# Optimization experiments

Hardware: AMD Instinct MI355X
Metric: run time of the kernel (lower is better)

The kernel has to match this reference:

```python
import jax, jax.numpy as jnp
import numpy as np

B, T, D, H = 2, 2048, 1024, 16
DK = D // H


def setup_inputs() -> dict:
    key = jax.random.key(0)
    ks = jax.random.split(key, 13)
    s = 1.0 / np.sqrt(D)
    return {
        "q": jax.random.normal(ks[0], (B, T, D), jnp.float32),
        "k": jax.random.normal(ks[1], (B, T, D), jnp.float32),
        "v": jax.random.normal(ks[2], (B, T, D), jnp.float32),
        "mask": jax.random.randint(ks[3], (B, T, T), 0, 2, jnp.int32),
        "Wq": jax.random.normal(ks[4], (D, D), jnp.float32) * s,
        "bq": jax.random.normal(ks[5], (D,), jnp.float32) * s,
        "Wk": jax.random.normal(ks[6], (D, D), jnp.float32) * s,
        "bk": jax.random.normal(ks[7], (D,), jnp.float32) * s,
        "Wv": jax.random.normal(ks[8], (D, D), jnp.float32) * s,
        "bv": jax.random.normal(ks[9], (D,), jnp.float32) * s,
        "Wo": jax.random.normal(ks[10], (D, D), jnp.float32) * s,
        "bo": jax.random.normal(ks[11], (D,), jnp.float32) * s,
    }


def reference(q, k, v, mask, Wq, bq, Wk, bk, Wv, bv, Wo, bo):
    # Linear projections (torch Linear: x @ W.T + b), split into heads.
    Q = (q @ Wq.T + bq).reshape(B, T, H, DK).transpose(0, 2, 1, 3)  # [B,H,Tq,dk]
    K = (k @ Wk.T + bk).reshape(B, T, H, DK).transpose(0, 2, 1, 3)
    V = (v @ Wv.T + bv).reshape(B, T, H, DK).transpose(0, 2, 1, 3)
    scores = jnp.einsum("bhqd,bhkd->bhqk", Q, K) / jnp.sqrt(jnp.float32(DK))
    # 3-dim mask path: mask==0 -> -1e9, broadcast over heads.
    scores = jnp.where(mask[:, None, :, :] == 0, jnp.float32(-1e9), scores)
    attn = jax.nn.softmax(scores, axis=-1)
    out = jnp.einsum("bhqk,bhkd->bhqd", attn, V)  # [B,H,Tq,dk]
    out = out.transpose(0, 2, 1, 3).reshape(B, T, D)
    return out @ Wo.T + bo
```

## Files before the change

### kernel.cpp

```cpp
#include <hip/hip_runtime.h>
#include <cstdint>
#include <cstddef>

#define TSEQ 2048
#define DMOD 1024
#define NHEAD 16
#define NBATCH 2
#define MT (NBATCH * TSEQ)
#define LOG2E 1.44269504088896340736f

typedef __attribute__((ext_vector_type(8))) __bf16 bf16x8;
typedef __attribute__((ext_vector_type(4))) float f32x4;
typedef __attribute__((ext_vector_type(8))) unsigned short u16x8;
typedef __attribute__((ext_vector_type(4))) unsigned short u16x4;
typedef __attribute__((ext_vector_type(4))) uint32_t u32x4;

__device__ __forceinline__ unsigned short f2bf(float f) {
  uint32_t u = __builtin_bit_cast(uint32_t, f);
  u += 0x7fffu + ((u >> 16) & 1u);
  return (unsigned short)(u >> 16);
}

__device__ __forceinline__ uint32_t cvt_pk_bf16(float a, float b) {
  uint32_t r;
  asm("v_cvt_pk_bf16_f32 %0, %1, %2" : "=v"(r) : "v"(a), "v"(b));
  return r;
}

__device__ __forceinline__ void gload_lds16(const void* g, const void* l) {
  auto gp = (const __attribute__((address_space(1))) uint32_t*)((uintptr_t)g);
  auto lp = (__attribute__((address_space(3))) uint32_t*)((uintptr_t)l);
  __builtin_amdgcn_global_load_lds(gp, lp, 16, 0, 0);
}

__global__ __launch_bounds__(256) void cvt_in(const float* __restrict__ q,
                                              const float* __restrict__ k,
                                              const float* __restrict__ v,
                                              unsigned short* __restrict__ dst) {
  const int y = blockIdx.y;
  const float* s = y == 0 ? q : (y == 1 ? k : v);
  const size_t i = ((size_t)blockIdx.x * 256 + threadIdx.x) * 4;
  const float4 t = *(const float4*)(s + i);
  u16x4 o;
  o[0] = f2bf(t.x); o[1] = f2bf(t.y); o[2] = f2bf(t.z); o[3] = f2bf(t.w);
  *(u16x4*)(dst + (size_t)y * MT * DMOD + i) = o;
}

__global__ __launch_bounds__(256) void cvt_w(const float* __restrict__ w0,
                                             const float* __restrict__ w1,
                                             const float* __restrict__ w2,
                                             const float* __restrict__ w3,
                                             unsigned short* __restrict__ dst) {
  const int y = blockIdx.y;
  const float* s = y == 0 ? w0 : (y == 1 ? w1 : (y == 2 ? w2 : w3));
  const size_t i = ((size_t)blockIdx.x * 256 + threadIdx.x) * 4;
  const float4 t = *(const float4*)(s + i);
  u16x4 o;
  o[0] = f2bf(t.x); o[1] = f2bf(t.y); o[2] = f2bf(t.z); o[3] = f2bf(t.w);
  *(u16x4*)(dst + (size_t)y * DMOD * DMOD + i) = o;
}

__global__ __launch_bounds__(256) void mask_bits(const int* __restrict__ m,
                                                 uint32_t* __restrict__ bits) {
  const int wg = (blockIdx.x * 256 + threadIdx.x) >> 6;
  const int lane = threadIdx.x & 63;
  const int v = m[(size_t)wg * 64 + lane];
  const unsigned long long b = __ballot(v != 0);
  if (lane == 0) *(uint2*)(bits + (size_t)wg * 2) = make_uint2((uint32_t)b, (uint32_t)(b >> 32));
}

__device__ __forceinline__ void store_c(unsigned short* C, size_t idx, float v) { C[idx] = f2bf(v); }
__device__ __forceinline__ void store_c(float* C, size_t idx, float v) { C[idx] = v; }

template <typename OT>
__global__ __launch_bounds__(256) void gemm_bt(const unsigned short* __restrict__ A0,
                                               const unsigned short* __restrict__ A1,
                                               const unsigned short* __restrict__ A2,
                                               const unsigned short* __restrict__ W0,
                                               const unsigned short* __restrict__ W1,
                                               const unsigned short* __restrict__ W2,
                                               const float* __restrict__ b0,
                                               const float* __restrict__ b1,
                                               const float* __restrict__ b2,
                                               OT* __restrict__ C0, OT* __restrict__ C1, OT* __restrict__ C2,
                                               float s0, float s1, float s2) {
  const int z = blockIdx.z;
  const unsigned short* A  = z == 0 ? A0 : (z == 1 ? A1 : A2);
  const unsigned short* Bw = z == 0 ? W0 : (z == 1 ? W1 : W2);
  const float* bias = z == 0 ? b0 : (z == 1 ? b1 : b2);
  OT* C = z == 0 ? C0 : (z == 1 ? C1 : C2);
  const float scale = z == 0 ? s0 : (z == 1 ? s1 : s2);

  __shared__ alignas(16) unsigned short As[128 * 32];
  __shared__ alignas(16) unsigned short Bs[128 * 32];
  const int tid = threadIdx.x;
  const int wid = tid >> 6;
  const int lane = tid & 63;
  const int lo = lane & 15, hi = lane >> 4;
  const int m0 = blockIdx.x * 128, n0 = blockIdx.y * 128;
  const int wr = wid >> 1, wc = wid & 1;
  f32x4 acc[4][4] = {};

  for (int k0 = 0; k0 < DMOD; k0 += 32) {
    __syncthreads();
#pragma unroll
    for (int i = 0; i < 2; ++i) {
      const int chunk = i * 256 + tid;
      const int row = chunk >> 2, c = chunk & 3;
      const int wb = (i * 256 + wid * 64) * 16;
      gload_lds16(A + (size_t)(m0 + row) * DMOD + k0 + c * 8, (const char*)As + wb);
      gload_lds16(Bw + (size_t)(n0 + row) * DMOD + k0 + c * 8, (const char*)Bs + wb);
    }
    __syncthreads();
    bf16x8 af[4], bfr[4];
#pragma unroll
    for (int m = 0; m < 4; ++m)
      af[m] = *(const bf16x8*)((const char*)As + (wr * 64 + m * 16 + lo) * 64 + hi * 16);
#pragma unroll
    for (int n = 0; n < 4; ++n)
      bfr[n] = *(const bf16x8*)((const char*)Bs + (wc * 64 + n * 16 + lo) * 64 + hi * 16);
#pragma unroll
    for (int m = 0; m < 4; ++m)
#pragma unroll
      for (int n = 0; n < 4; ++n)
        acc[m][n] = __builtin_amdgcn_mfma_f32_16x16x32_bf16(af[m], bfr[n], acc[m][n], 0, 0, 0);
  }

#pragma unroll
  for (int n = 0; n < 4; ++n) {
    const int col = n0 + wc * 64 + n * 16 + lo;
    const float bv = bias[col];
#pragma unroll
    for (int m = 0; m < 4; ++m) {
      const int row = m0 + wr * 64 + m * 16 + hi * 4;
#pragma unroll
      for (int r = 0; r < 4; ++r)
        store_c(C, (size_t)(row + r) * DMOD + col, (acc[m][n][r] + bv) * scale);
    }
  }
}

__global__ __launch_bounds__(256) void transpose_v(const unsigned short* __restrict__ Vp,
                                                   unsigned short* __restrict__ Vt) {
  __shared__ alignas(16) unsigned short tile[64][72];
  const int tid = threadIdx.x;
  const int bt0 = blockIdx.x * 64;
  const int h = blockIdx.y;
  const int b = bt0 >> 11;
  const int t0 = bt0 & (TSEQ - 1);
#pragma unroll
  for (int i = 0; i < 2; ++i) {
    const int chunk = i * 256 + tid;
    const int row = chunk >> 3, c = chunk & 7;
    *(uint4*)((char*)&tile[row][0] + c * 16) =
        *(const uint4*)(Vp + (size_t)(bt0 + row) * DMOD + h * 64 + c * 8);
  }
  __syncthreads();
#pragma unroll
  for (int i = 0; i < 2; ++i) {
    const int chunk = i * 256 + tid;
    const int dk = chunk >> 3, c = chunk & 7;
    u16x8 o;
#pragma unroll
    for (int j = 0; j < 8; ++j) {
      const int x = c * 8 + j;
      const int kl = (x & 32) | ((x & 24) >> 1) | ((x & 4) << 2) | (x & 3);
      o[j] = tile[kl][dk];
    }
    *(u16x8*)(Vt + ((size_t)(b * NHEAD + h) * 64 + dk) * TSEQ + t0 + c * 8) = o;
  }
}

__global__ __launch_bounds__(512, 4) void attn_kernel(const unsigned short* __restrict__ Qp,
                                                      const unsigned short* __restrict__ Kp,
                                                      const unsigned short* __restrict__ Vt,
                                                      const uint32_t* __restrict__ mbits,
                                                      unsigned short* __restrict__ AO) {
  __shared__ alignas(16) unsigned short Ks[2][128 * 64];
  __shared__ alignas(16) unsigned short Vs[2][64 * 128];
  const int tid = threadIdx.x;
  const int w = tid >> 6, lane = tid & 63;
  const int lo = lane & 15, hi = lane >> 4;
  const int f = blockIdx.x;
  const int swz = (f & 7) * 64 + (f >> 3);
  const int q0 = (swz & 15) * 128;
  const int h = (swz >> 4) & 15;
  const int b = swz >> 8;

  bf16x8 qf[2];
  {
    const unsigned short* qsrc =
        Qp + (size_t)(b * TSEQ + q0 + w * 16 + lo) * DMOD + h * 64 + hi * 8;
    qf[0] = *(const bf16x8*)qsrc;
    qf[1] = *(const bf16x8*)(qsrc + 32);
  }

  bf16x8 ones;
  {
    u32x4 od;
    od[0] = 0x3F803F80u; od[1] = 0x3F803F80u; od[2] = 0x3F803F80u; od[3] = 0x3F803F80u;
    ones = __builtin_bit_cast(bf16x8, od);
  }

  f32x4 o_acc[4] = {};
  f32x4 l_acc = {};

  const size_t kbase = (size_t)(b * TSEQ) * DMOD + h * 64;
  const size_t vbase = (size_t)(b * NHEAD + h) * 64 * TSEQ;
  const uint32_t* mrow = mbits + (size_t)(b * TSEQ + q0 + w * 16 + lo) * 64;

  auto stage = [&](int buf, int kt2) {
#pragma unroll
    for (int i = 0; i < 2; ++i) {
      const int chunk = i * 512 + tid;
      const int wb = chunk * 16;
      {
        const int row = chunk >> 3, c = (chunk & 7) ^ (row & 7);
        gload_lds16(Kp + kbase + (size_t)(kt2 * 128 + row) * DMOD + c * 8,
                    (const char*)Ks[buf] + wb);
      }
      {
        const int row = chunk >> 4, c = (chunk & 15) ^ (row & 7);
        gload_lds16(Vt + vbase + (size_t)row * TSEQ + kt2 * 128 + c * 8,
                    (const char*)Vs[buf] + wb);
      }
    }
  };

  const int NT = TSEQ / 128;
  stage(0, 0);
  uint4 mw = *(const uint4*)(mrow);
  __syncthreads();

  for (int kt = 0; kt < NT; ++kt) {
    const int cur = kt & 1;
    uint4 mw_next = mw;
    if (kt + 1 < NT) {
      stage(cur ^ 1, kt + 1);
      mw_next = *(const uint4*)(mrow + (kt + 1) * 4);
    }

    const char* ksb = (const char*)Ks[cur];
    f32x4 s[8];
    __builtin_amdgcn_s_setprio(1);
#pragma unroll
    for (int ct = 0; ct < 8; ++ct) {
      const int kcol = ct * 16 + lo;
      const char* kb8 = ksb + kcol * 128;
      bf16x8 kf0 = *(const bf16x8*)(kb8 + ((hi ^ (kcol & 7)) * 16));
      bf16x8 kf1 = *(const bf16x8*)(kb8 + (((4 + hi) ^ (kcol & 7)) * 16));
      f32x4 zz = {0.f, 0.f, 0.f, 0.f};
      s[ct] = __builtin_amdgcn_mfma_f32_16x16x32_bf16(kf0, qf[0], zz, 0, 0, 0);
      s[ct] = __builtin_amdgcn_mfma_f32_16x16x32_bf16(kf1, qf[1], s[ct], 0, 0, 0);
    }
    __builtin_amdgcn_s_setprio(0);

    {
      uint32_t mwa[4] = {mw.x, mw.y, mw.z, mw.w};
#pragma unroll
      for (int i = 0; i < 4; ++i) {
        const uint32_t tw = mwa[i] >> (hi * 4);
#pragma unroll
        for (int r = 0; r < 4; ++r) {
          if (((tw >> r) & 1u) == 0u) s[2 * i][r] = -1e9f;
          if (((tw >> (16 + r)) & 1u) == 0u) s[2 * i + 1][r] = -1e9f;
        }
      }
    }
#pragma unroll
    for (int ct = 0; ct < 8; ++ct) {
      s[ct][0] = __builtin_exp2f(s[ct][0]);
      s[ct][1] = __builtin_exp2f(s[ct][1]);
      s[ct][2] = __builtin_exp2f(s[ct][2]);
      s[ct][3] = __builtin_exp2f(s[ct][3]);
    }

    bf16x8 pf[4];
#pragma unroll
    for (int c = 0; c < 4; ++c) {
      u32x4 pd;
      pd[0] = cvt_pk_bf16(s[2 * c][0], s[2 * c][1]);
      pd[1] = cvt_pk_bf16(s[2 * c][2], s[2 * c][3]);
      pd[2] = cvt_pk_bf16(s[2 * c + 1][0], s[2 * c + 1][1]);
      pd[3] = cvt_pk_bf16(s[2 * c + 1][2], s[2 * c + 1][3]);
      pf[c] = __builtin_bit_cast(bf16x8, pd);
    }

    const char* vsb = (const char*)Vs[cur];
    __builtin_amdgcn_s_setprio(1);
#pragma unroll
    for (int vt = 0; vt < 4; ++vt) {
      const int dk = vt * 16 + lo;
      const char* vb8 = vsb + dk * 256;
      const int sw = dk & 7;
#pragma unroll
      for (int c = 0; c < 4; ++c) {
        bf16x8 vf = *(const bf16x8*)(vb8 + (((c * 4 + hi) ^ sw) * 16));
        o_acc[vt] = __builtin_amdgcn_mfma_f32_16x16x32_bf16(pf[c], vf, o_acc[vt], 0, 0, 0);
      }
    }
#pragma unroll
    for (int c = 0; c < 4; ++c)
      l_acc = __builtin_amdgcn_mfma_f32_16x16x32_bf16(pf[c], ones, l_acc, 0, 0, 0);
    __builtin_amdgcn_s_setprio(0);

    __syncthreads();
    mw = mw_next;
  }

#pragma unroll
  for (int r = 0; r < 4; ++r) {
    const float rl = 1.0f / l_acc[r];
    const size_t orow = (size_t)(b * TSEQ + q0 + w * 16 + hi * 4 + r) * DMOD + h * 64;
#pragma unroll
    for (int vt = 0; vt < 4; ++vt)
      AO[orow + vt * 16 + lo] = f2bf(o_acc[vt][r] * rl);
  }
}

extern "C" void kernel_launch(void* const* d_in, const int* in_sizes, int n_in,
                              void* d_out, int out_size, void* d_ws, size_t ws_size,
                              hipStream_t stream) {
  const float* q  = (const float*)d_in[0];
  const float* k  = (const float*)d_in[1];
  const float* v  = (const float*)d_in[2];
  const int* mask = (const int*)d_in[3];
  const float* Wq = (const float*)d_in[4];
  const float* bq = (const float*)d_in[5];
  const float* Wk = (const float*)d_in[6];
  const float* bk = (const float*)d_in[7];
  const float* Wv = (const float*)d_in[8];
  const float* bv = (const float*)d_in[9];
  const float* Wo = (const float*)d_in[10];
  const float* bo = (const float*)d_in[11];
  float* out = (float*)d_out;

  char* ws = (char*)d_ws;
  const size_t SZ_BT = (size_t)MT * DMOD * 2;
  const size_t SZ_W  = (size_t)DMOD * DMOD * 2;

  unsigned short* qb  = (unsigned short*)(ws + 0);
  unsigned short* kb  = (unsigned short*)(ws + SZ_BT);
  unsigned short* vb  = (unsigned short*)(ws + 2 * SZ_BT);
  unsigned short* Qp  = (unsigned short*)(ws + 3 * SZ_BT);
  unsigned short* Kp  = (unsigned short*)(ws + 4 * SZ_BT);
  unsigned short* Vp  = (unsigned short*)(ws + 5 * SZ_BT);
  unsigned short* Wqb = (unsigned short*)(ws + 6 * SZ_BT);
  unsigned short* Wob = (unsigned short*)(ws + 6 * SZ_BT + 3 * SZ_W);
  unsigned short* Vt  = vb;
  unsigned short* AO  = qb;
  uint32_t*       mbits = (uint32_t*)kb;

  const int nBT = MT * DMOD;
  const int nW  = DMOD * DMOD;

  cvt_in<<<dim3(nBT / 1024, 3), 256, 0, stream>>>(q, k, v, qb);
  cvt_w<<<dim3(nW / 1024, 4), 256, 0, stream>>>(Wq, Wk, Wv, Wo, Wqb);

  const float qs = 0.125f * LOG2E;
  gemm_bt<unsigned short><<<dim3(MT / 128, DMOD / 128, 3), 256, 0, stream>>>(
      qb, kb, vb, Wqb, Wqb + nW, Wqb + 2 * nW, bq, bk, bv, Qp, Kp, Vp, qs, 1.0f, 1.0f);

  mask_bits<<<(NBATCH * TSEQ * TSEQ) / (64 * 4), 256, 0, stream>>>(mask, mbits);

  transpose_v<<<dim3(MT / 64, NHEAD), 256, 0, stream>>>(Vp, Vt);

  attn_kernel<<<dim3(512), 512, 0, stream>>>(Qp, Kp, Vt, mbits, AO);

  gemm_bt<float><<<dim3(MT / 128, DMOD / 128, 1), 256, 0, stream>>>(
      AO, AO, AO, Wob, Wob, Wob, bo, bo, bo, out, out, out, 1.0f, 1.0f, 1.0f);
}
```

Baseline: 163.6 us.

## Expand mask to byte masks, precompute LDS offsets, merge conversions, shrink output GEMM tile

The bit-packed mask is replaced by a per-lane byte-expanded mask. The attention kernel applies it with a perm-and-AND on the packed bf16 probabilities, so the per-element compare-and-select is gone. LDS fragment offsets and global staging pointers are precomputed outside the loop. The two conversion kernels are merged into one launch, and the output projection GEMM uses 64-row tiles to launch more blocks. In exchange, the mask buffer becomes 8x larger (more memory traffic) and many more conversion blocks exit early.

```diff
diff --git a/kernel.cpp b/kernel.cpp
--- a/kernel.cpp
+++ b/kernel.cpp
@@ -33,46 +33,53 @@
   __builtin_amdgcn_global_load_lds(gp, lp, 16, 0, 0);
 }
 
-__global__ __launch_bounds__(256) void cvt_in(const float* __restrict__ q,
-                                              const float* __restrict__ k,
-                                              const float* __restrict__ v,
-                                              unsigned short* __restrict__ dst) {
+__global__ __launch_bounds__(256) void cvt_all(const float* __restrict__ q,
+                                               const float* __restrict__ k,
+                                               const float* __restrict__ v,
+                                               const float* __restrict__ w0,
+                                               const float* __restrict__ w1,
+                                               const float* __restrict__ w2,
+                                               const float* __restrict__ w3,
+                                               unsigned short* __restrict__ din,
+                                               unsigned short* __restrict__ dw) {
   const int y = blockIdx.y;
-  const float* s = y == 0 ? q : (y == 1 ? k : v);
+  const float* s;
+  unsigned short* d;
+  size_t n;
+  if (y < 3) {
+    s = y == 0 ? q : (y == 1 ? k : v);
+    d = din + (size_t)y * MT * DMOD;
+    n = (size_t)MT * DMOD;
+  } else {
+    s = y == 3 ? w0 : (y == 4 ? w1 : (y == 5 ? w2 : w3));
+    d = dw + (size_t)(y - 3) * DMOD * DMOD;
+    n = (size_t)DMOD * DMOD;
+  }
   const size_t i = ((size_t)blockIdx.x * 256 + threadIdx.x) * 4;
+  if (i >= n) return;
   const float4 t = *(const float4*)(s + i);
   u16x4 o;
   o[0] = f2bf(t.x); o[1] = f2bf(t.y); o[2] = f2bf(t.z); o[3] = f2bf(t.w);
-  *(u16x4*)(dst + (size_t)y * MT * DMOD + i) = o;
-}
-
-__global__ __launch_bounds__(256) void cvt_w(const float* __restrict__ w0,
-                                             const float* __restrict__ w1,
-                                             const float* __restrict__ w2,
-                                             const float* __restrict__ w3,
-                                             unsigned short* __restrict__ dst) {
-  const int y = blockIdx.y;
-  const float* s = y == 0 ? w0 : (y == 1 ? w1 : (y == 2 ? w2 : w3));
-  const size_t i = ((size_t)blockIdx.x * 256 + threadIdx.x) * 4;
-  const float4 t = *(const float4*)(s + i);
-  u16x4 o;
-  o[0] = f2bf(t.x); o[1] = f2bf(t.y); o[2] = f2bf(t.z); o[3] = f2bf(t.w);
-  *(u16x4*)(dst + (size_t)y * DMOD * DMOD + i) = o;
-}
-
-__global__ __launch_bounds__(256) void mask_bits(const int* __restrict__ m,
-                                                 uint32_t* __restrict__ bits) {
-  const int wg = (blockIdx.x * 256 + threadIdx.x) >> 6;
-  const int lane = threadIdx.x & 63;
-  const int v = m[(size_t)wg * 64 + lane];
-  const unsigned long long b = __ballot(v != 0);
-  if (lane == 0) *(uint2*)(bits + (size_t)wg * 2) = make_uint2((uint32_t)b, (uint32_t)(b >> 32));
+  *(u16x4*)(d + i) = o;
+}
+
+__global__ __launch_bounds__(256) void mask_exp(const int* __restrict__ m,
+                                                uint32_t* __restrict__ mx) {
+  const size_t W = (size_t)blockIdx.x * 256 + threadIdx.x;
+  const int hi = (int)((W >> 3) & 3), ct = (int)(W & 7);
+  const size_t bqkt = W >> 5;
+  const int kt = (int)(bqkt & 15);
+  const size_t bq = bqkt >> 4;
+  const int4 mm = *(const int4*)(m + bq * TSEQ + kt * 128 + ct * 16 + hi * 4);
+  const uint32_t o = (mm.x ? 0xFFu : 0u) | (mm.y ? 0xFF00u : 0u) |
+                     (mm.z ? 0xFF0000u : 0u) | (mm.w ? 0xFF000000u : 0u);
+  mx[W] = o;
 }
 
 __device__ __forceinline__ void store_c(unsigned short* C, size_t idx, float v) { C[idx] = f2bf(v); }
 __device__ __forceinline__ void store_c(float* C, size_t idx, float v) { C[idx] = v; }
 
-template <typename OT>
+template <typename OT, int MF>
 __global__ __launch_bounds__(256) void gemm_bt(const unsigned short* __restrict__ A0,
                                                const unsigned short* __restrict__ A1,
                                                const unsigned short* __restrict__ A2,
@@ -84,6 +91,7 @@
                                                const float* __restrict__ b2,
                                                OT* __restrict__ C0, OT* __restrict__ C1, OT* __restrict__ C2,
                                                float s0, float s1, float s2) {
+  constexpr int BM = MF * 32;
   const int z = blockIdx.z;
   const unsigned short* A  = z == 0 ? A0 : (z == 1 ? A1 : A2);
   const unsigned short* Bw = z == 0 ? W0 : (z == 1 ? W1 : W2);
@@ -91,15 +99,15 @@
   OT* C = z == 0 ? C0 : (z == 1 ? C1 : C2);
   const float scale = z == 0 ? s0 : (z == 1 ? s1 : s2);
 
-  __shared__ alignas(16) unsigned short As[128 * 32];
+  __shared__ alignas(16) unsigned short As[BM * 32];
   __shared__ alignas(16) unsigned short Bs[128 * 32];
   const int tid = threadIdx.x;
   const int wid = tid >> 6;
   const int lane = tid & 63;
   const int lo = lane & 15, hi = lane >> 4;
-  const int m0 = blockIdx.x * 128, n0 = blockIdx.y * 128;
+  const int m0 = blockIdx.x * BM, n0 = blockIdx.y * 128;
   const int wr = wid >> 1, wc = wid & 1;
-  f32x4 acc[4][4] = {};
+  f32x4 acc[MF][4] = {};
 
   for (int k0 = 0; k0 < DMOD; k0 += 32) {
     __syncthreads();
@@ -108,19 +116,20 @@
       const int chunk = i * 256 + tid;
       const int row = chunk >> 2, c = chunk & 3;
       const int wb = (i * 256 + wid * 64) * 16;
-      gload_lds16(A + (size_t)(m0 + row) * DMOD + k0 + c * 8, (const char*)As + wb);
+      if (i < MF / 2)
+        gload_lds16(A + (size_t)(m0 + row) * DMOD + k0 + c * 8, (const char*)As + wb);
       gload_lds16(Bw + (size_t)(n0 + row) * DMOD + k0 + c * 8, (const char*)Bs + wb);
     }
     __syncthreads();
-    bf16x8 af[4], bfr[4];
-#pragma unroll
-    for (int m = 0; m < 4; ++m)
-      af[m] = *(const bf16x8*)((const char*)As + (wr * 64 + m * 16 + lo) * 64 + hi * 16);
+    bf16x8 af[MF], bfr[4];
+#pragma unroll
+    for (int m = 0; m < MF; ++m)
+      af[m] = *(const bf16x8*)((const char*)As + (wr * (MF * 16) + m * 16 + lo) * 64 + hi * 16);
 #pragma unroll
     for (int n = 0; n < 4; ++n)
       bfr[n] = *(const bf16x8*)((const char*)Bs + (wc * 64 + n * 16 + lo) * 64 + hi * 16);
 #pragma unroll
-    for (int m = 0; m < 4; ++m)
+    for (int m = 0; m < MF; ++m)
 #pragma unroll
       for (int n = 0; n < 4; ++n)
         acc[m][n] = __builtin_amdgcn_mfma_f32_16x16x32_bf16(af[m], bfr[n], acc[m][n], 0, 0, 0);
@@ -131,8 +140,8 @@
     const int col = n0 + wc * 64 + n * 16 + lo;
     const float bv = bias[col];
 #pragma unroll
-    for (int m = 0; m < 4; ++m) {
-      const int row = m0 + wr * 64 + m * 16 + hi * 4;
+    for (int m = 0; m < MF; ++m) {
+      const int row = m0 + wr * (MF * 16) + m * 16 + hi * 4;
 #pragma unroll
       for (int r = 0; r < 4; ++r)
         store_c(C, (size_t)(row + r) * DMOD + col, (acc[m][n][r] + bv) * scale);
@@ -174,7 +183,7 @@
 __global__ __launch_bounds__(512, 4) void attn_kernel(const unsigned short* __restrict__ Qp,
                                                       const unsigned short* __restrict__ Kp,
                                                       const unsigned short* __restrict__ Vt,
-                                                      const uint32_t* __restrict__ mbits,
+                                                      const uint32_t* __restrict__ mx,
                                                       unsigned short* __restrict__ AO) {
   __shared__ alignas(16) unsigned short Ks[2][128 * 64];
   __shared__ alignas(16) unsigned short Vs[2][64 * 128];
@@ -207,66 +216,70 @@
 
   const size_t kbase = (size_t)(b * TSEQ) * DMOD + h * 64;
   const size_t vbase = (size_t)(b * NHEAD + h) * 64 * TSEQ;
-  const uint32_t* mrow = mbits + (size_t)(b * TSEQ + q0 + w * 16 + lo) * 64;
-
-  auto stage = [&](int buf, int kt2) {
-#pragma unroll
-    for (int i = 0; i < 2; ++i) {
-      const int chunk = i * 512 + tid;
-      const int wb = chunk * 16;
-      {
-        const int row = chunk >> 3, c = (chunk & 7) ^ (row & 7);
-        gload_lds16(Kp + kbase + (size_t)(kt2 * 128 + row) * DMOD + c * 8,
-                    (const char*)Ks[buf] + wb);
-      }
-      {
-        const int row = chunk >> 4, c = (chunk & 15) ^ (row & 7);
-        gload_lds16(Vt + vbase + (size_t)row * TSEQ + kt2 * 128 + c * 8,
-                    (const char*)Vs[buf] + wb);
-      }
-    }
+
+  const int c0 = tid, c1 = 512 + tid;
+  const unsigned short* kp0 = Kp + kbase + (size_t)(c0 >> 3) * DMOD + ((c0 & 7) ^ ((c0 >> 3) & 7)) * 8;
+  const unsigned short* kp1 = Kp + kbase + (size_t)(c1 >> 3) * DMOD + ((c1 & 7) ^ ((c1 >> 3) & 7)) * 8;
+  const unsigned short* vp0 = Vt + vbase + (size_t)(c0 >> 4) * TSEQ + ((c0 & 15) ^ ((c0 >> 4) & 7)) * 8;
+  const unsigned short* vp1 = Vt + vbase + (size_t)(c1 >> 4) * TSEQ + ((c1 & 15) ^ ((c1 >> 4) & 7)) * 8;
+  const uint32_t* mp = mx + (size_t)(b * TSEQ + q0 + w * 16 + lo) * 512 + hi * 8;
+  const int wb0 = c0 * 16, wb1 = c1 * 16;
+
+  int koffA[8], koffB[8];
+#pragma unroll
+  for (int ct = 0; ct < 8; ++ct) {
+    const int kcol = ct * 16 + lo;
+    koffA[ct] = kcol * 128 + ((hi ^ (kcol & 7)) * 16);
+    koffB[ct] = kcol * 128 + (((4 + hi) ^ (kcol & 7)) * 16);
+  }
+  int voff[4][4];
+#pragma unroll
+  for (int vt = 0; vt < 4; ++vt) {
+    const int dk = vt * 16 + lo;
+#pragma unroll
+    for (int c = 0; c < 4; ++c) voff[vt][c] = dk * 256 + (((c * 4 + hi) ^ (dk & 7)) * 16);
+  }
+
+  auto stage = [&](int buf) {
+    gload_lds16(kp0, (const char*)Ks[buf] + wb0);
+    gload_lds16(kp1, (const char*)Ks[buf] + wb1);
+    gload_lds16(vp0, (const char*)Vs[buf] + wb0);
+    gload_lds16(vp1, (const char*)Vs[buf] + wb1);
+    kp0 += (size_t)128 * DMOD; kp1 += (size_t)128 * DMOD;
+    vp0 += 128; vp1 += 128;
   };
 
+  const uint32_t selA = 0x01010000u, selB = 0x03030202u;
   const int NT = TSEQ / 128;
-  stage(0, 0);
-  uint4 mw = *(const uint4*)(mrow);
+
+  uint4 mc0 = *(const uint4*)mp, mc1 = *(const uint4*)(mp + 4);
+  mp += 32;
+  stage(0);
   __syncthreads();
 
   for (int kt = 0; kt < NT; ++kt) {
-    const int cur = kt & 1;
-    uint4 mw_next = mw;
+    uint4 mn0 = mc0, mn1 = mc1;
     if (kt + 1 < NT) {
-      stage(cur ^ 1, kt + 1);
-      mw_next = *(const uint4*)(mrow + (kt + 1) * 4);
-    }
-
-    const char* ksb = (const char*)Ks[cur];
+      mn0 = *(const uint4*)mp;
+      mn1 = *(const uint4*)(mp + 4);
+      mp += 32;
+      stage((kt + 1) & 1);
+    }
+
+    const char* ksb = (const char*)Ks[kt & 1];
+    const char* vsb = (const char*)Vs[kt & 1];
     f32x4 s[8];
     __builtin_amdgcn_s_setprio(1);
 #pragma unroll
     for (int ct = 0; ct < 8; ++ct) {
-      const int kcol = ct * 16 + lo;
-      const char* kb8 = ksb + kcol * 128;
-      bf16x8 kf0 = *(const bf16x8*)(kb8 + ((hi ^ (kcol & 7)) * 16));
-      bf16x8 kf1 = *(const bf16x8*)(kb8 + (((4 + hi) ^ (kcol & 7)) * 16));
+      bf16x8 kf0 = *(const bf16x8*)(ksb + koffA[ct]);
+      bf16x8 kf1 = *(const bf16x8*)(ksb + koffB[ct]);
       f32x4 zz = {0.f, 0.f, 0.f, 0.f};
       s[ct] = __builtin_amdgcn_mfma_f32_16x16x32_bf16(kf0, qf[0], zz, 0, 0, 0);
       s[ct] = __builtin_amdgcn_mfma_f32_16x16x32_bf16(kf1, qf[1], s[ct], 0, 0, 0);
     }
     __builtin_amdgcn_s_setprio(0);
 
-    {
-      uint32_t mwa[4] = {mw.x, mw.y, mw.z, mw.w};
-#pragma unroll
-      for (int i = 0; i < 4; ++i) {
-        const uint32_t tw = mwa[i] >> (hi * 4);
-#pragma unroll
-        for (int r = 0; r < 4; ++r) {
-          if (((tw >> r) & 1u) == 0u) s[2 * i][r] = -1e9f;
-          if (((tw >> (16 + r)) & 1u) == 0u) s[2 * i + 1][r] = -1e9f;
-        }
-      }
-    }
 #pragma unroll
     for (int ct = 0; ct < 8; ++ct) {
       s[ct][0] = __builtin_exp2f(s[ct][0]);
@@ -278,24 +291,22 @@
     bf16x8 pf[4];
 #pragma unroll
     for (int c = 0; c < 4; ++c) {
+      const uint32_t We = c == 0 ? mc0.x : (c == 1 ? mc0.z : (c == 2 ? mc1.x : mc1.z));
+      const uint32_t Wo = c == 0 ? mc0.y : (c == 1 ? mc0.w : (c == 2 ? mc1.y : mc1.w));
       u32x4 pd;
-      pd[0] = cvt_pk_bf16(s[2 * c][0], s[2 * c][1]);
-      pd[1] = cvt_pk_bf16(s[2 * c][2], s[2 * c][3]);
-      pd[2] = cvt_pk_bf16(s[2 * c + 1][0], s[2 * c + 1][1]);
-      pd[3] = cvt_pk_bf16(s[2 * c + 1][2], s[2 * c + 1][3]);
+      pd[0] = cvt_pk_bf16(s[2 * c][0], s[2 * c][1]) & __builtin_amdgcn_perm(We, We, selA);
+      pd[1] = cvt_pk_bf16(s[2 * c][2], s[2 * c][3]) & __builtin_amdgcn_perm(We, We, selB);
+      pd[2] = cvt_pk_bf16(s[2 * c + 1][0], s[2 * c + 1][1]) & __builtin_amdgcn_perm(Wo, Wo, selA);
+      pd[3] = cvt_pk_bf16(s[2 * c + 1][2], s[2 * c + 1][3]) & __builtin_amdgcn_perm(Wo, Wo, selB);
       pf[c] = __builtin_bit_cast(bf16x8, pd);
     }
 
-    const char* vsb = (const char*)Vs[cur];
     __builtin_amdgcn_s_setprio(1);
 #pragma unroll
     for (int vt = 0; vt < 4; ++vt) {
-      const int dk = vt * 16 + lo;
-      const char* vb8 = vsb + dk * 256;
-      const int sw = dk & 7;
 #pragma unroll
       for (int c = 0; c < 4; ++c) {
-        bf16x8 vf = *(const bf16x8*)(vb8 + (((c * 4 + hi) ^ sw) * 16));
+        bf16x8 vf = *(const bf16x8*)(vsb + voff[vt][c]);
         o_acc[vt] = __builtin_amdgcn_mfma_f32_16x16x32_bf16(pf[c], vf, o_acc[vt], 0, 0, 0);
       }
     }
@@ -305,7 +316,7 @@
     __builtin_amdgcn_s_setprio(0);
 
     __syncthreads();
-    mw = mw_next;
+    mc0 = mn0; mc1 = mn1;
   }
 
 #pragma unroll
@@ -349,24 +360,23 @@
   unsigned short* Wob = (unsigned short*)(ws + 6 * SZ_BT + 3 * SZ_W);
   unsigned short* Vt  = vb;
   unsigned short* AO  = qb;
-  uint32_t*       mbits = (uint32_t*)kb;
+  uint32_t*       mx  = (uint32_t*)kb;
 
   const int nBT = MT * DMOD;
   const int nW  = DMOD * DMOD;
 
-  cvt_in<<<dim3(nBT / 1024, 3), 256, 0, stream>>>(q, k, v, qb);
-  cvt_w<<<dim3(nW / 1024, 4), 256, 0, stream>>>(Wq, Wk, Wv, Wo, Wqb);
+  cvt_all<<<dim3(nBT / 1024, 7), 256, 0, stream>>>(q, k, v, Wq, Wk, Wv, Wo, qb, Wqb);
 
   const float qs = 0.125f * LOG2E;
-  gemm_bt<unsigned short><<<dim3(MT / 128, DMOD / 128, 3), 256, 0, stream>>>(
+  gemm_bt<unsigned short, 4><<<dim3(MT / 128, DMOD / 128, 3), 256, 0, stream>>>(
       qb, kb, vb, Wqb, Wqb + nW, Wqb + 2 * nW, bq, bk, bv, Qp, Kp, Vp, qs, 1.0f, 1.0f);
 
-  mask_bits<<<(NBATCH * TSEQ * TSEQ) / (64 * 4), 256, 0, stream>>>(mask, mbits);
+  mask_exp<<<(NBATCH * TSEQ * 16 * 32) / 256, 256, 0, stream>>>(mask, mx);
 
   transpose_v<<<dim3(MT / 64, NHEAD), 256, 0, stream>>>(Vp, Vt);
 
-  attn_kernel<<<dim3(512), 512, 0, stream>>>(Qp, Kp, Vt, mbits, AO);
-
-  gemm_bt<float><<<dim3(MT / 128, DMOD / 128, 1), 256, 0, stream>>>(
+  attn_kernel<<<dim3(512), 512, 0, stream>>>(Qp, Kp, Vt, mx, AO);
+
+  gemm_bt<float, 2><<<dim3(MT / 64, DMOD / 128, 1), 256, 0, stream>>>(
       AO, AO, AO, Wob, Wob, Wob, bo, bo, bo, out, out, out, 1.0f, 1.0f, 1.0f);
 }
```

Result: faster. 154.7 us (-5.4%).
